# Optimization experiments

Hardware: AMD Instinct MI355X
Metric: run time of the kernel (lower is better)

Reference implementation:

```python
import jax, jax.numpy as jnp
import numpy as np

D_MODEL = 2048
K_DIM = 128
V_DIM = 128
H = 16
B = 1
S = 2048
SCALE_BASE = 512.0
THETA = 10000.0
EPS = 1e-5


def setup_inputs() -> dict:
    key = jax.random.key(0)
    ks = jax.random.split(key, 11)
    lin = lambda k, i, o: jax.random.normal(k, (i, o), jnp.float32) * 0.02
    return {
        "x": jax.random.normal(ks[0], (B, S, D_MODEL), jnp.float32),
        "Wq": lin(ks[1], D_MODEL, K_DIM * H), "bq": jnp.zeros((K_DIM * H,), jnp.float32),
        "Wk": lin(ks[2], D_MODEL, K_DIM * H), "bk": jnp.zeros((K_DIM * H,), jnp.float32),
        "Wv": lin(ks[3], D_MODEL, V_DIM * H), "bv": jnp.zeros((V_DIM * H,), jnp.float32),
        "Wg": lin(ks[4], D_MODEL, V_DIM * H), "bg": jnp.zeros((V_DIM * H,), jnp.float32),
        "Wo": lin(ks[5], V_DIM * H, D_MODEL), "bo": jnp.zeros((D_MODEL,), jnp.float32),
    }


def _rotate_half(x):
    # interleaved pairs: (x0, x1, x2, x3, ...) -> (-x1, x0, -x3, x2, ...)
    xr = x.reshape(*x.shape[:-1], -1, 2)
    x1, x2 = xr[..., 0], xr[..., 1]
    return jnp.stack((-x2, x1), axis=-1).reshape(x.shape)


def _rope_xpos(q, k, seq_len, dim):
    pos = jnp.arange(seq_len, dtype=jnp.float32)
    inv_freq = 1.0 / (THETA ** (jnp.arange(0, dim, 2, dtype=jnp.float32) / dim))
    freqs = jnp.repeat(pos[:, None] * inv_freq[None, :], 2, axis=-1)  # (S, dim)
    cos, sin = jnp.cos(freqs), jnp.sin(freqs)
    sbase = (jnp.arange(0, dim, 2, dtype=jnp.float32) + 0.4 * dim) / (1.4 * dim)
    power = (pos - seq_len // 2) / SCALE_BASE
    scale = jnp.repeat(sbase[None, :] ** power[:, None], 2, axis=-1)  # (S, dim)
    q = (q * cos + _rotate_half(q) * sin) * scale
    k = (k * cos + _rotate_half(k) * sin) / scale
    return q, k


def reference(x, Wq, bq, Wk, bk, Wv, bv, Wg, bg, Wo, bo):
    Bb, Ss, Dd = x.shape
    heads = lambda t: t.reshape(Bb, Ss, H, -1).transpose(0, 2, 1, 3)  # (B,H,S,d)
    q = heads(x @ Wq + bq)
    k = heads(x @ Wk + bk)
    v = heads(x @ Wv + bv)
    q, k = _rope_xpos(q, k, Ss, K_DIM)
    # per-head decay gamma_h = 1 - 2^{-5-h}
    gamma = 1.0 - 2.0 ** (-5.0 - jnp.arange(H, dtype=jnp.float32))
    pos = jnp.arange(Ss, dtype=jnp.float32)
    pm = pos[:, None] - pos[None, :]  # (S,S)
    decay_mask = jnp.where(pm >= 0, gamma[:, None, None] ** jnp.maximum(pm, 0.0), 0.0)  # (H,S,S)
    scores = jnp.einsum('bhid,bhjd->bhij', q, k) * decay_mask
    ret = jnp.einsum('bhij,bhjd->bhid', scores, v)  # (B,H,S,V_DIM)
    # concat heads and GroupNorm (num_groups=H, affine=False) over flattened rows
    concat = ret.transpose(0, 2, 1, 3).reshape(Bb * Ss, H, V_DIM)
    mu = concat.mean(-1, keepdims=True)
    var = ((concat - mu) ** 2).mean(-1, keepdims=True)
    gn = ((concat - mu) / jnp.sqrt(var + EPS)).reshape(Bb, Ss, H * V_DIM)
    out = (jax.nn.silu(x @ Wg + bg) * gn) @ Wo + bo
    return out
```

## Files before the change

kernel.cpp:

```cpp
#include <hip/hip_runtime.h>
#include <hip/hip_bf16.h>

#define S 2048
#define DM 2048
#define H 16
#define HD 128

using bf16 = __hip_bfloat16;
typedef __attribute__((ext_vector_type(8))) short bf16x8;
typedef __attribute__((ext_vector_type(8))) unsigned short u16x8;
typedef __attribute__((ext_vector_type(4))) float f32x4;

__device__ __forceinline__ unsigned short f2bu(float f) {
  bf16 b = __float2bfloat16(f);
  union { bf16 b; unsigned short u; } cv; cv.b = b; return cv.u;
}
__device__ __forceinline__ float bu2f(unsigned short u) {
  union { bf16 b; unsigned short u; } cv; cv.u = u; return __bfloat162float(cv.b);
}

__device__ __forceinline__ void async_copy16(const void* g, void* l) {
  __builtin_amdgcn_global_load_lds(
      (const __attribute__((address_space(1))) void*)g,
      (__attribute__((address_space(3))) void*)l, 16, 0, 0);
}

__global__ __launch_bounds__(256) void wtrans_kernel(
    const float* __restrict__ s0, const float* __restrict__ s1, const float* __restrict__ s2,
    const float* __restrict__ s3, const float* __restrict__ s4,
    unsigned short* __restrict__ d0, unsigned short* __restrict__ d1, unsigned short* __restrict__ d2,
    unsigned short* __restrict__ d3, unsigned short* __restrict__ d4,
    const float* __restrict__ x, unsigned short* __restrict__ xb) {
  __shared__ float tile[64][65];
  int z = blockIdx.z;
  int tid = threadIdx.x;
  int by = blockIdx.y * 64;
  int bx = blockIdx.x * 64;
  int r0 = tid >> 4;
  int c0 = (tid & 15) * 4;
  if (z == 5) {
#pragma unroll
    for (int i = 0; i < 4; i++) {
      int row = by + r0 + i * 16;
      float4 t = *(const float4*)(x + (size_t)row * DM + bx + c0);
      ushort4 o;
      o.x = f2bu(t.x); o.y = f2bu(t.y); o.z = f2bu(t.z); o.w = f2bu(t.w);
      *(ushort4*)(xb + (size_t)row * DM + bx + c0) = o;
    }
    return;
  }
  const float* src = z == 0 ? s0 : z == 1 ? s1 : z == 2 ? s2 : z == 3 ? s3 : s4;
  unsigned short* dst = z == 0 ? d0 : z == 1 ? d1 : z == 2 ? d2 : z == 3 ? d3 : d4;
#pragma unroll
  for (int i = 0; i < 4; i++) {
    int row = r0 + i * 16;
    float4 t = *(const float4*)(src + (size_t)(by + row) * DM + bx + c0);
    tile[row][c0 + 0] = t.x; tile[row][c0 + 1] = t.y;
    tile[row][c0 + 2] = t.z; tile[row][c0 + 3] = t.w;
  }
  __syncthreads();
#pragma unroll
  for (int i = 0; i < 4; i++) {
    int nrow = r0 + i * 16;
    ushort4 o;
    o.x = f2bu(tile[c0 + 0][nrow]);
    o.y = f2bu(tile[c0 + 1][nrow]);
    o.z = f2bu(tile[c0 + 2][nrow]);
    o.w = f2bu(tile[c0 + 3][nrow]);
    *(ushort4*)(dst + (size_t)(bx + nrow) * DM + by + c0) = o;
  }
}

__device__ __forceinline__ void stage_half(const unsigned short* gbase, char* ldsbase, int tid) {
#pragma unroll
  for (int r = 0; r < 2; r++) {
    int a = r * 8192 + tid * 16;
    int row = a >> 7;
    int cb = (a & 127) ^ ((row & 7) << 4);
    async_copy16((const unsigned char*)(gbase + (size_t)row * DM) + cb, ldsbase + a);
  }
}

#define LDB4(dst, base, kkofs)                                                                     \
  _Pragma("unroll") for (int nt = 0; nt < 4; ++nt) {                                               \
    int lr = blr0 + nt * 16;                                                                       \
    dst[nt] = *(const bf16x8*)((base) + bhalf + lr * 128 + (((kkofs) + quad * 16) ^ ((lr & 7) << 4))); \
  }
#define LDA4(dst, base, kkofs)                                                                     \
  _Pragma("unroll") for (int mt = 0; mt < 4; ++mt) {                                               \
    int lr = mt * 32 + wm * 16 + r16;                                                              \
    dst[mt] = *(const bf16x8*)((base) + lr * 128 + (((kkofs) + quad * 16) ^ ((lr & 7) << 4)));     \
  }
#define MFMA16(accbase, af, bf)                                                                    \
  _Pragma("unroll") for (int mt = 0; mt < 4; ++mt)                                                 \
    _Pragma("unroll") for (int nt = 0; nt < 4; ++nt)                                               \
      acc[accbase + mt][nt] = __builtin_amdgcn_mfma_f32_16x16x32_bf16(af[mt], bf[nt], acc[accbase + mt][nt], 0, 0, 0);
#define PHASE_SYNC()                                            \
  __builtin_amdgcn_s_barrier();                                 \
  asm volatile("s_waitcnt lgkmcnt(0)" ::: "memory");            \
  __builtin_amdgcn_sched_barrier(0);

__global__ __launch_bounds__(512, 2) void gemm_qkvg_kernel(
    const unsigned short* __restrict__ A, const unsigned short* __restrict__ Bm,
    const float* __restrict__ bias0, const float* __restrict__ bias1,
    const float* __restrict__ bias2, const float* __restrict__ bias3,
    unsigned short* __restrict__ C0, unsigned short* __restrict__ C1,
    unsigned short* __restrict__ Vt, unsigned short* __restrict__ C3) {
  __shared__ alignas(16) char smem[131072];
  char* sA = smem;
  char* sB = smem + 65536;
  int tid = threadIdx.x;
  int wg = blockIdx.y * 32 + blockIdx.x;
  int swz = (wg & 7) * 32 + (wg >> 3);
  int bm = (swz >> 5) * 256;
  int bn = (swz & 31) * 256;
  int wid = tid >> 6, lane = tid & 63;
  int wm = wid >> 2, wn = wid & 3;
  int r16 = lane & 15, quad = lane >> 4;
  f32x4 acc[8][4] = {};
  const int bhalf = (wn >> 1) << 14;
  const int blr0 = ((wn & 1) << 6) + r16;

  stage_half(Bm + (size_t)bn * DM, sB, tid);
  stage_half(Bm + (size_t)(bn + 128) * DM, sB + 16384, tid);
  stage_half(A + (size_t)bm * DM, sA, tid);
  stage_half(A + (size_t)(bm + 128) * DM, sA + 16384, tid);
  stage_half(Bm + (size_t)bn * DM + 64, sB + 32768, tid);
  stage_half(Bm + (size_t)(bn + 128) * DM + 64, sB + 49152, tid);
  asm volatile("s_waitcnt vmcnt(6)" ::: "memory");
  __builtin_amdgcn_s_barrier();

  for (int u = 0; u < 16; ++u) {
    const bool more = u < 15;
    const int k1 = (2 * u + 1) * 64;
    const int k2 = (2 * u + 2) * 64;
    const int k3 = (2 * u + 3) * 64;
    bf16x8 a0[4], a1[4], b0[4], b1[4];

    LDB4(b0, sB, 0)
    LDA4(a0, sA, 0)
    stage_half(A + (size_t)bm * DM + k1, sA + 32768, tid);
    PHASE_SYNC()
    __builtin_amdgcn_s_setprio(1);
    MFMA16(0, a0, b0)
    __builtin_amdgcn_s_setprio(0);

    LDB4(b1, sB, 64)
    LDA4(a1, sA, 64)
    stage_half(A + (size_t)(bm + 128) * DM + k1, sA + 49152, tid);
    asm volatile("s_waitcnt vmcnt(8)" ::: "memory");
    PHASE_SYNC()
    __builtin_amdgcn_s_setprio(1);
    MFMA16(0, a1, b1)
    __builtin_amdgcn_s_setprio(0);

    LDA4(a0, sA + 16384, 0)
    if (more) stage_half(Bm + (size_t)bn * DM + k2, sB, tid);
    PHASE_SYNC()
    __builtin_amdgcn_s_setprio(1);
    MFMA16(4, a0, b0)
    __builtin_amdgcn_s_setprio(0);

    LDA4(a1, sA + 16384, 64)
    if (more) {
      stage_half(Bm + (size_t)(bn + 128) * DM + k2, sB + 16384, tid);
      asm volatile("s_waitcnt vmcnt(6)" ::: "memory");
    } else {
      asm volatile("s_waitcnt vmcnt(2)" ::: "memory");
    }
    PHASE_SYNC()
    __builtin_amdgcn_s_setprio(1);
    MFMA16(4, a1, b1)
    __builtin_amdgcn_s_setprio(0);

    LDB4(b0, sB + 32768, 0)
    LDA4(a0, sA + 32768, 0)
    if (more) stage_half(A + (size_t)bm * DM + k2, sA, tid);
    PHASE_SYNC()
    __builtin_amdgcn_s_setprio(1);
    MFMA16(0, a0, b0)
    __builtin_amdgcn_s_setprio(0);

    LDB4(b1, sB + 32768, 64)
    LDA4(a1, sA + 32768, 64)
    if (more) {
      stage_half(A + (size_t)(bm + 128) * DM + k2, sA + 16384, tid);
      asm volatile("s_waitcnt vmcnt(8)" ::: "memory");
    } else {
      asm volatile("s_waitcnt vmcnt(0)" ::: "memory");
    }
    PHASE_SYNC()
    __builtin_amdgcn_s_setprio(1);
    MFMA16(0, a1, b1)
    __builtin_amdgcn_s_setprio(0);

    LDA4(a0, sA + 32768 + 16384, 0)
    if (more) stage_half(Bm + (size_t)bn * DM + k3, sB + 32768, tid);
    PHASE_SYNC()
    __builtin_amdgcn_s_setprio(1);
    MFMA16(4, a0, b0)
    __builtin_amdgcn_s_setprio(0);

    LDA4(a1, sA + 32768 + 16384, 64)
    if (more) {
      stage_half(Bm + (size_t)(bn + 128) * DM + k3, sB + 49152, tid);
      asm volatile("s_waitcnt vmcnt(6)" ::: "memory");
    }
    PHASE_SYNC()
    __builtin_amdgcn_s_setprio(1);
    MFMA16(4, a1, b1)
    __builtin_amdgcn_s_setprio(0);
  }

  int ch = bn >> 11;
  const float* bp = ch == 0 ? bias0 : ch == 1 ? bias1 : ch == 2 ? bias2 : bias3;
  int lcb = bn & 2047;
  if (ch == 2) {
#pragma unroll
    for (int nt = 0; nt < 4; ++nt) {
      int lc = lcb + wn * 64 + nt * 16 + r16;
      float bv = bp[lc];
#pragma unroll
      for (int mt = 0; mt < 8; ++mt) {
        int m0 = bm + (mt >> 2) * 128 + (mt & 3) * 32 + wm * 16 + quad * 4;
        ushort4 o;
        o.x = f2bu(acc[mt][nt][0] + bv);
        o.y = f2bu(acc[mt][nt][1] + bv);
        o.z = f2bu(acc[mt][nt][2] + bv);
        o.w = f2bu(acc[mt][nt][3] + bv);
        *(ushort4*)(Vt + (size_t)lc * DM + m0) = o;
      }
    }
  } else {
    unsigned short* Cp = ch == 0 ? C0 : ch == 1 ? C1 : C3;
#pragma unroll
    for (int nt = 0; nt < 4; ++nt) {
      int lc = lcb + wn * 64 + nt * 16 + r16;
      float bv = bp[lc];
#pragma unroll
      for (int mt = 0; mt < 8; ++mt) {
        int m0 = bm + (mt >> 2) * 128 + (mt & 3) * 32 + wm * 16 + quad * 4;
#pragma unroll
        for (int rr = 0; rr < 4; ++rr)
          Cp[(size_t)(m0 + rr) * DM + lc] = f2bu(acc[mt][nt][rr] + bv);
      }
    }
  }
}

__device__ __forceinline__ void stage_o(const unsigned short* gA, const unsigned short* gB,
                                        char* dA, char* dB, int tid) {
#pragma unroll
  for (int r = 0; r < 4; r++) {
    int a = r * 4096 + tid * 16;
    int row = a >> 7;
    int cb = (a & 127) ^ ((row & 7) << 4);
    async_copy16((const unsigned char*)(gA + (size_t)row * DM) + cb, dA + a);
  }
#pragma unroll
  for (int r = 0; r < 2; r++) {
    int a = r * 4096 + tid * 16;
    int row = a >> 7;
    int cb = (a & 127) ^ ((row & 7) << 4);
    async_copy16((const unsigned char*)(gB + (size_t)row * DM) + cb, dB + a);
  }
}

__global__ __launch_bounds__(256) void gemm_out_kernel(
    const unsigned short* __restrict__ A, const unsigned short* __restrict__ Bp,
    const float* __restrict__ bias, float* __restrict__ C) {
  __shared__ alignas(16) char sA[2][16384];
  __shared__ alignas(16) char sB[2][8192];
  int tid = threadIdx.x;
  int wg = blockIdx.y * 32 + blockIdx.x;
  int swz = (wg & 7) * 64 + (wg >> 3);
  int bm = (swz >> 5) * 128;
  int bn = (swz & 31) * 64;
  int wid = tid >> 6, lane = tid & 63;
  int wm = wid >> 1, wn = wid & 1;
  int r16 = lane & 15, quad = lane >> 4;
  f32x4 acc[4][2] = {};

  stage_o(A + (size_t)bm * DM, Bp + (size_t)bn * DM, sA[0], sB[0], tid);
  asm volatile("s_waitcnt vmcnt(0)" ::: "memory");
  __builtin_amdgcn_s_barrier();

  for (int t = 0; t < 32; ++t) {
    int cur = t & 1;
    bool more = t < 31;
    int kn = (t + 1) * 64;
    if (more)
      stage_o(A + (size_t)bm * DM + kn, Bp + (size_t)bn * DM + kn, sA[cur ^ 1], sB[cur ^ 1], tid);
#pragma unroll
    for (int kk = 0; kk < 2; kk++) {
      bf16x8 af[4], bfr[2];
#pragma unroll
      for (int mt = 0; mt < 4; mt++) {
        int row = wm * 64 + mt * 16 + r16;
        af[mt] = *(const bf16x8*)(sA[cur] + row * 128 + ((kk * 64 + quad * 16) ^ ((row & 7) << 4)));
      }
#pragma unroll
      for (int nt = 0; nt < 2; nt++) {
        int row = wn * 32 + nt * 16 + r16;
        bfr[nt] = *(const bf16x8*)(sB[cur] + row * 128 + ((kk * 64 + quad * 16) ^ ((row & 7) << 4)));
      }
#pragma unroll
      for (int mt = 0; mt < 4; mt++)
#pragma unroll
        for (int nt = 0; nt < 2; nt++)
          acc[mt][nt] = __builtin_amdgcn_mfma_f32_16x16x32_bf16(af[mt], bfr[nt], acc[mt][nt], 0, 0, 0);
    }
    asm volatile("s_waitcnt vmcnt(0)" ::: "memory");
    __builtin_amdgcn_s_barrier();
  }
#pragma unroll
  for (int nt = 0; nt < 2; nt++) {
    int n = bn + wn * 32 + nt * 16 + r16;
    float bv = bias[n];
#pragma unroll
    for (int mt = 0; mt < 4; mt++) {
      int m0 = bm + wm * 64 + mt * 16 + quad * 4;
#pragma unroll
      for (int r = 0; r < 4; r++)
        C[(size_t)(m0 + r) * DM + n] = acc[mt][nt][r] + bv;
    }
  }
}

__global__ __launch_bounds__(256) void rope_kernel(unsigned short* __restrict__ q,
                                                   unsigned short* __restrict__ k) {
  int idx = blockIdx.x * 256 + threadIdx.x;
  int s = idx >> 10;
  int p = idx & 1023;
  int t = p & 63;
  int head = p >> 6;
  int col = (head << 7) + (t << 1);
  size_t off = (size_t)s * DM + col;
  float ang = (float)s * exp2f((float)(-2 * t) * (13.287712379549449f / 128.0f));
  float sn, cs;
  sincosf(ang, &sn, &cs);
  float sb = ((float)(2 * t) + 51.2f) * (1.0f / 179.2f);
  float power = ((float)s - 1024.0f) * (1.0f / 512.0f);
  float scale = exp2f(power * log2f(sb));
  float l2g = log2f(1.0f - exp2f((float)(-5 - head)));
  float qsc = scale * exp2f((float)s * l2g);
  float ksc = (1.0f / scale) * exp2f(-(float)s * l2g);
  unsigned int qu = *(unsigned int*)(q + off);
  float a = bu2f(qu & 0xffff), b = bu2f(qu >> 16);
  float qa = (a * cs - b * sn) * qsc;
  float qb2 = (b * cs + a * sn) * qsc;
  *(unsigned int*)(q + off) = (unsigned int)f2bu(qa) | ((unsigned int)f2bu(qb2) << 16);
  unsigned int ku = *(unsigned int*)(k + off);
  float c2 = bu2f(ku & 0xffff), d2 = bu2f(ku >> 16);
  float ka = (c2 * cs - d2 * sn) * ksc;
  float kb2 = (d2 * cs + c2 * sn) * ksc;
  *(unsigned int*)(k + off) = (unsigned int)f2bu(ka) | ((unsigned int)f2bu(kb2) << 16);
}

__device__ __forceinline__ void stage_kv(const unsigned short* __restrict__ k,
                                         const unsigned short* __restrict__ vt,
                                         int h, int J0, unsigned char* dK,
                                         unsigned char* dV, int tid) {
#pragma unroll
  for (int r = 0; r < 4; r++) {
    int a = r * 4096 + tid * 16;
    int rowk = a >> 8;
    int cbk = (a & 255) ^ ((rowk & 7) << 4);
    async_copy16((const unsigned char*)(k + (size_t)(J0 + rowk) * DM + h * HD) + cbk, dK + a);
    int rowv = a >> 7;
    int cbv = (a & 127) ^ ((rowv & 7) << 4);
    async_copy16((const unsigned char*)(vt + (size_t)(h * HD + rowv) * DM + J0) + cbv, dV + a);
  }
}

__global__ __launch_bounds__(256) void retention_kernel(
    const unsigned short* __restrict__ q, const unsigned short* __restrict__ k,
    const unsigned short* __restrict__ vt, const unsigned short* __restrict__ g,
    unsigned short* __restrict__ y) {
  __shared__ alignas(16) unsigned char sK[2][16384];
  __shared__ alignas(16) unsigned char sV[2][16384];
  __shared__ alignas(16) unsigned char Plds[8192];
  int bx = blockIdx.x;
  int hi = bx >> 8;
  int h = ((bx >> 5) & 7) | (hi << 3);
  int ib = hi ? (bx & 31) : (31 - (bx & 31));
  int I = ib << 6;
  int tid = threadIdx.x, wid = tid >> 6, lane = tid & 63;
  int r16 = lane & 15, quad = lane >> 4;
  bf16x8 aQ[4];
  size_t qrow = (size_t)(I + wid * 16 + r16);
#pragma unroll
  for (int kk = 0; kk < 4; kk++)
    aQ[kk] = *(const bf16x8*)(q + qrow * DM + h * HD + kk * 32 + quad * 8);
  f32x4 acc[8] = {};
  unsigned char* Pw = Plds + wid * 2048;
  stage_kv(k, vt, h, 0, sK[0], sV[0], tid);
  for (int J0 = 0; J0 <= I; J0 += 64) {
    int cur = (J0 >> 6) & 1;
    bool more = (J0 + 64) <= I;
    if (more) stage_kv(k, vt, h, J0 + 64, sK[cur ^ 1], sV[cur ^ 1], tid);
    if (more) { asm volatile("s_waitcnt vmcnt(8)" ::: "memory"); }
    else      { asm volatile("s_waitcnt vmcnt(0)" ::: "memory"); }
    __builtin_amdgcn_s_barrier();
    const unsigned char* sKc = sK[cur];
    const unsigned char* sVc = sV[cur];
    f32x4 sf[4] = {};
#pragma unroll
    for (int nt = 0; nt < 4; nt++) {
      int row = nt * 16 + r16;
#pragma unroll
      for (int kk = 0; kk < 4; kk++) {
        bf16x8 bK = *(const bf16x8*)(sKc + row * 256 + ((kk * 64 + quad * 16) ^ ((row & 7) << 4)));
        sf[nt] = __builtin_amdgcn_mfma_f32_16x16x32_bf16(aQ[kk], bK, sf[nt], 0, 0, 0);
      }
    }
    bool diag = (J0 == I);
#pragma unroll
    for (int nt = 0; nt < 4; nt++) {
      int j = nt * 16 + r16;
#pragma unroll
      for (int r = 0; r < 4; r++) {
        int ii = wid * 16 + quad * 4 + r;
        float pv = sf[nt][r];
        if (diag && (ii - j) < 0) pv = 0.0f;
        int pr = quad * 4 + r;
        int pcb = (nt * 16 + r16) * 2;
        *(unsigned short*)(Pw + pr * 128 + (pcb ^ ((pr & 7) << 4))) = f2bu(pv);
      }
    }
#pragma unroll
    for (int kk2 = 0; kk2 < 2; kk2++) {
      int cb = kk2 * 64 + quad * 16;
      bf16x8 aP = *(const bf16x8*)(Pw + r16 * 128 + (cb ^ ((r16 & 7) << 4)));
#pragma unroll
      for (int nt2 = 0; nt2 < 8; nt2++) {
        int row = nt2 * 16 + r16;
        bf16x8 bV = *(const bf16x8*)(sVc + row * 128 + ((kk2 * 64 + quad * 16) ^ ((row & 7) << 4)));
        acc[nt2] = __builtin_amdgcn_mfma_f32_16x16x32_bf16(aP, bV, acc[nt2], 0, 0, 0);
      }
    }
    __builtin_amdgcn_s_barrier();
  }
#pragma unroll
  for (int r = 0; r < 4; r++) {
    float sum = 0.0f, sq = 0.0f;
#pragma unroll
    for (int nt2 = 0; nt2 < 8; nt2++) {
      float v = acc[nt2][r];
      sum += v; sq += v * v;
    }
#pragma unroll
    for (int o = 1; o <= 8; o <<= 1) {
      sum += __shfl_xor(sum, o, 64);
      sq += __shfl_xor(sq, o, 64);
    }
    float mean = sum * 0.0078125f;
    float var = sq * 0.0078125f - mean * mean;
    float rstd = rsqrtf(var + 1e-5f);
    int i = I + wid * 16 + quad * 4 + r;
    size_t rowbase = (size_t)i * DM + h * HD;
#pragma unroll
    for (int nt2 = 0; nt2 < 8; nt2++) {
      int col = nt2 * 16 + r16;
      float gv = bu2f(g[rowbase + col]);
      float sg = gv / (1.0f + expf(-gv));
      float yv = sg * (acc[nt2][r] - mean) * rstd;
      y[rowbase + col] = f2bu(yv);
    }
  }
}

extern "C" void kernel_launch(void* const* d_in, const int* in_sizes, int n_in,
                              void* d_out, int out_size, void* d_ws, size_t ws_size,
                              hipStream_t stream) {
  (void)in_sizes; (void)n_in; (void)out_size; (void)ws_size;
  const float* x  = (const float*)d_in[0];
  const float* Wq = (const float*)d_in[1];
  const float* bq = (const float*)d_in[2];
  const float* Wk = (const float*)d_in[3];
  const float* bk = (const float*)d_in[4];
  const float* Wv = (const float*)d_in[5];
  const float* bv = (const float*)d_in[6];
  const float* Wg = (const float*)d_in[7];
  const float* bg = (const float*)d_in[8];
  const float* Wo = (const float*)d_in[9];
  const float* bo = (const float*)d_in[10];

  char* ws = (char*)d_ws;
  const size_t MB = 1ull << 20;
  unsigned short* xb   = (unsigned short*)(ws + 0 * MB);
  unsigned short* wcat = (unsigned short*)(ws + 8 * MB);
  unsigned short* wto  = (unsigned short*)(ws + 40 * MB);
  unsigned short* qb   = (unsigned short*)(ws + 48 * MB);
  unsigned short* kb   = (unsigned short*)(ws + 56 * MB);
  unsigned short* gb   = (unsigned short*)(ws + 72 * MB);
  unsigned short* vt   = (unsigned short*)(ws + 80 * MB);
  unsigned short* yb   = (unsigned short*)(ws + 104 * MB);

  wtrans_kernel<<<dim3(32, 32, 6), 256, 0, stream>>>(
      Wq, Wk, Wv, Wg, Wo,
      wcat, wcat + (size_t)2048 * DM, wcat + (size_t)4096 * DM, wcat + (size_t)6144 * DM, wto,
      x, xb);
  gemm_qkvg_kernel<<<dim3(32, 8), 512, 0, stream>>>(
      xb, wcat, bq, bk, bv, bg, qb, kb, vt, gb);
  rope_kernel<<<8192, 256, 0, stream>>>(qb, kb);
  retention_kernel<<<512, 256, 0, stream>>>(qb, kb, vt, gb, yb);
  gemm_out_kernel<<<dim3(32, 16), 256, 0, stream>>>(yb, wto, bo, (float*)d_out);
}
```

Measured before the change: 169.7 us.

## Replace double-buffered async GEMM pipeline with single-buffer load-wait-compute loop

The QKVG projection GEMM drops its double-buffered LDS ping-pong with interleaved async global-to-LDS prefetch. Each K tile is now staged into a single 64KB buffer, the kernel waits for all loads, computes, then barriers. This halves shared memory and removes many per-phase barriers, but global load latency is no longer overlapped with MFMA work. It may be a simplification or a test of whether the lower LDS footprint helps occupancy.

Result: slower. 198.1 us (+16.7%).

```diff
diff --git a/kernel.cpp b/kernel.cpp
--- a/kernel.cpp
+++ b/kernel.cpp
@@ -95,10 +95,6 @@
   _Pragma("unroll") for (int mt = 0; mt < 4; ++mt)                                                 \
     _Pragma("unroll") for (int nt = 0; nt < 4; ++nt)                                               \
       acc[accbase + mt][nt] = __builtin_amdgcn_mfma_f32_16x16x32_bf16(af[mt], bf[nt], acc[accbase + mt][nt], 0, 0, 0);
-#define PHASE_SYNC()                                            \
-  __builtin_amdgcn_s_barrier();                                 \
-  asm volatile("s_waitcnt lgkmcnt(0)" ::: "memory");            \
-  __builtin_amdgcn_sched_barrier(0);
 
 __global__ __launch_bounds__(512, 2) void gemm_qkvg_kernel(
     const unsigned short* __restrict__ A, const unsigned short* __restrict__ Bm,
@@ -106,9 +102,9 @@
     const float* __restrict__ bias2, const float* __restrict__ bias3,
     unsigned short* __restrict__ C0, unsigned short* __restrict__ C1,
     unsigned short* __restrict__ Vt, unsigned short* __restrict__ C3) {
-  __shared__ alignas(16) char smem[131072];
+  __shared__ alignas(16) char smem[65536];
   char* sA = smem;
-  char* sB = smem + 65536;
+  char* sB = smem + 32768;
   int tid = threadIdx.x;
   int wg = blockIdx.y * 32 + blockIdx.x;
   int swz = (wg & 7) * 32 + (wg >> 3);
@@ -121,95 +117,44 @@
   const int bhalf = (wn >> 1) << 14;
   const int blr0 = ((wn & 1) << 6) + r16;
 
-  stage_half(Bm + (size_t)bn * DM, sB, tid);
-  stage_half(Bm + (size_t)(bn + 128) * DM, sB + 16384, tid);
-  stage_half(A + (size_t)bm * DM, sA, tid);
-  stage_half(A + (size_t)(bm + 128) * DM, sA + 16384, tid);
-  stage_half(Bm + (size_t)bn * DM + 64, sB + 32768, tid);
-  stage_half(Bm + (size_t)(bn + 128) * DM + 64, sB + 49152, tid);
-  asm volatile("s_waitcnt vmcnt(6)" ::: "memory");
-  __builtin_amdgcn_s_barrier();
-
-  for (int u = 0; u < 16; ++u) {
-    const bool more = u < 15;
-    const int k1 = (2 * u + 1) * 64;
-    const int k2 = (2 * u + 2) * 64;
-    const int k3 = (2 * u + 3) * 64;
+  for (int t = 0; t < 32; ++t) {
+    const int kt = t * 64;
+    stage_half(Bm + (size_t)bn * DM + kt, sB, tid);
+    stage_half(Bm + (size_t)(bn + 128) * DM + kt, sB + 16384, tid);
+    stage_half(A + (size_t)bm * DM + kt, sA, tid);
+    stage_half(A + (size_t)(bm + 128) * DM + kt, sA + 16384, tid);
+    asm volatile("s_waitcnt vmcnt(0)" ::: "memory");
+    __builtin_amdgcn_s_barrier();
+
     bf16x8 a0[4], a1[4], b0[4], b1[4];
-
     LDB4(b0, sB, 0)
     LDA4(a0, sA, 0)
-    stage_half(A + (size_t)bm * DM + k1, sA + 32768, tid);
-    PHASE_SYNC()
+    LDB4(b1, sB, 64)
+    LDA4(a1, sA, 64)
+    asm volatile("s_waitcnt lgkmcnt(8)" ::: "memory");
+    __builtin_amdgcn_sched_barrier(0);
     __builtin_amdgcn_s_setprio(1);
     MFMA16(0, a0, b0)
     __builtin_amdgcn_s_setprio(0);
-
-    LDB4(b1, sB, 64)
-    LDA4(a1, sA, 64)
-    stage_half(A + (size_t)(bm + 128) * DM + k1, sA + 49152, tid);
-    asm volatile("s_waitcnt vmcnt(8)" ::: "memory");
-    PHASE_SYNC()
+    LDA4(a0, sA + 16384, 0)
+    asm volatile("s_waitcnt lgkmcnt(4)" ::: "memory");
+    __builtin_amdgcn_sched_barrier(0);
     __builtin_amdgcn_s_setprio(1);
     MFMA16(0, a1, b1)
     __builtin_amdgcn_s_setprio(0);
-
-    LDA4(a0, sA + 16384, 0)
-    if (more) stage_half(Bm + (size_t)bn * DM + k2, sB, tid);
-    PHASE_SYNC()
+    LDA4(a1, sA + 16384, 64)
+    asm volatile("s_waitcnt lgkmcnt(4)" ::: "memory");
+    __builtin_amdgcn_sched_barrier(0);
     __builtin_amdgcn_s_setprio(1);
     MFMA16(4, a0, b0)
     __builtin_amdgcn_s_setprio(0);
-
-    LDA4(a1, sA + 16384, 64)
-    if (more) {
-      stage_half(Bm + (size_t)(bn + 128) * DM + k2, sB + 16384, tid);
-      asm volatile("s_waitcnt vmcnt(6)" ::: "memory");
-    } else {
-      asm volatile("s_waitcnt vmcnt(2)" ::: "memory");
-    }
-    PHASE_SYNC()
+    asm volatile("s_waitcnt lgkmcnt(0)" ::: "memory");
+    __builtin_amdgcn_sched_barrier(0);
     __builtin_amdgcn_s_setprio(1);
     MFMA16(4, a1, b1)
     __builtin_amdgcn_s_setprio(0);
 
-    LDB4(b0, sB + 32768, 0)
-    LDA4(a0, sA + 32768, 0)
-    if (more) stage_half(A + (size_t)bm * DM + k2, sA, tid);
-    PHASE_SYNC()
-    __builtin_amdgcn_s_setprio(1);
-    MFMA16(0, a0, b0)
-    __builtin_amdgcn_s_setprio(0);
-
-    LDB4(b1, sB + 32768, 64)
-    LDA4(a1, sA + 32768, 64)
-    if (more) {
-      stage_half(A + (size_t)(bm + 128) * DM + k2, sA + 16384, tid);
-      asm volatile("s_waitcnt vmcnt(8)" ::: "memory");
-    } else {
-      asm volatile("s_waitcnt vmcnt(0)" ::: "memory");
-    }
-    PHASE_SYNC()
-    __builtin_amdgcn_s_setprio(1);
-    MFMA16(0, a1, b1)
-    __builtin_amdgcn_s_setprio(0);
-
-    LDA4(a0, sA + 32768 + 16384, 0)
-    if (more) stage_half(Bm + (size_t)bn * DM + k3, sB + 32768, tid);
-    PHASE_SYNC()
-    __builtin_amdgcn_s_setprio(1);
-    MFMA16(4, a0, b0)
-    __builtin_amdgcn_s_setprio(0);
-
-    LDA4(a1, sA + 32768 + 16384, 64)
-    if (more) {
-      stage_half(Bm + (size_t)(bn + 128) * DM + k3, sB + 49152, tid);
-      asm volatile("s_waitcnt vmcnt(6)" ::: "memory");
-    }
-    PHASE_SYNC()
-    __builtin_amdgcn_s_setprio(1);
-    MFMA16(4, a1, b1)
-    __builtin_amdgcn_s_setprio(0);
+    __builtin_amdgcn_s_barrier();
   }
 
   int ch = bn >> 11;
```
